# Kernel tuning notes

Measured on AMD Instinct MI355X. Metric: run time of the kernel, lower is better.

The kernel has to match this reference:

```python
import jax, jax.numpy as jnp
import numpy as np

B, C, H, W = 32, 256, 56, 56
G, K, RED = 2, 7, 4
BN_EPS = 1e-5


def _conv2d(x, w, pad, groups=1, bias=None):
    # x: (N, Cin, H, W), w: (Cout, Cin/groups, kh, kw)
    y = jax.lax.conv_general_dilated(
        x, w, window_strides=(1, 1), padding=[(pad, pad), (pad, pad)],
        dimension_numbers=("NCHW", "OIHW", "NCHW"), feature_group_count=groups)
    if bias is not None:
        y = y + bias[None, :, None, None]
    return y


def setup_inputs() -> dict:
    key = jax.random.key(0)
    ks = jax.random.split(key, 5)
    return {
        "x": jax.random.normal(ks[0], (B, C, H, W), jnp.float32),
        "w_dyn": jax.random.normal(ks[1], (G, C, K, K), jnp.float32) * 0.02,
        "proj1_w": jax.random.normal(ks[2], (C // RED, C, 3, 3), jnp.float32) * 0.02,
        "bn_gamma": jnp.ones((C // RED,), jnp.float32),
        "bn_beta": jnp.zeros((C // RED,), jnp.float32),
        "proj2_w": jax.random.normal(ks[3], (C * G, C // RED, 3, 3), jnp.float32) * 0.02,
        "proj2_b": jnp.zeros((C * G,), jnp.float32),
    }


def reference(x, w_dyn, proj1_w, bn_gamma, bn_beta, proj2_w, proj2_b):
    b, c, h, w = x.shape
    # AdaptiveAvgPool2d((K, K)); H, W divisible by K -> exact mean over (H//K, W//K) windows
    pooled = x.reshape(b, c, K, h // K, K, w // K).mean(axis=(3, 5))  # (B, C, K, K)
    # proj: Conv3x3 (no bias, BN follows) -> BN (inference: mean=0, var=1) -> GELU -> Conv3x3
    hmid = _conv2d(pooled, proj1_w, pad=1)
    hmid = hmid * (bn_gamma / jnp.sqrt(1.0 + BN_EPS))[None, :, None, None] + bn_beta[None, :, None, None]
    hmid = jax.nn.gelu(hmid, approximate=False)
    scale = _conv2d(hmid, proj2_w, pad=1, bias=proj2_b)  # (B, G*C, K, K)
    scale = jax.nn.softmax(scale.reshape(b, G, c, K, K), axis=1)
    # per-sample dynamic depthwise kernel: softmax-weighted mix of G kernel banks
    dyn_w = jnp.einsum("bgckl,gckl->bckl", scale, w_dyn)  # (B, C, K, K)
    # depthwise conv with per-sample weights: groups = B*C
    y = _conv2d(x.reshape(1, b * c, h, w), dyn_w.reshape(b * c, 1, K, K),
                pad=K // 2, groups=b * c)
    return y.reshape(b, c, h, w)
```

## Files before the change

kernel.cpp:

```cpp
#include <hip/hip_runtime.h>
#include <math.h>

#define BB 32
#define CC 256
#define HH 56
#define WW 56
#define KP 49
#define CMID 64
#define HW 3136

__global__ __launch_bounds__(256) void pre_kernel(const float* __restrict__ x,
                                                  const float* __restrict__ w1,
                                                  const float* __restrict__ w2,
                                                  float* __restrict__ pooled,
                                                  float* __restrict__ w1t,
                                                  float* __restrict__ w2t) {
    int bid = blockIdx.x;
    if (bid < 2048) {
        int wv = threadIdx.x >> 6, lane = threadIdx.x & 63;
        int g = bid * 4 + wv;
        if (lane < KP) {
            int ko = lane / 7, kw = lane - ko * 7;
            const float* base = x + (size_t)g * HW + (ko * 8) * WW + kw * 8;
            float s = 0.f;
            #pragma unroll
            for (int r = 0; r < 8; ++r) {
                float4 a = *(const float4*)(base + r * WW);
                float4 b4 = *(const float4*)(base + r * WW + 4);
                s += a.x + a.y + a.z + a.w + b4.x + b4.y + b4.z + b4.w;
            }
            pooled[(size_t)g * KP + lane] = s * (1.f / 64.f);
        }
        return;
    }
    __shared__ float t[64][65];
    int r = threadIdx.x >> 6, c = threadIdx.x & 63;
    if (bid < 2048 + 36) {
        int ct0 = (bid - 2048) * 64;
        #pragma unroll
        for (int i = 0; i < 16; ++i)
            t[r + 4 * i][c] = w1[(size_t)(r + 4 * i) * 2304 + ct0 + c];
        __syncthreads();
        #pragma unroll
        for (int i = 0; i < 16; ++i)
            w1t[(size_t)(ct0 + r + 4 * i) * 64 + c] = t[c][r + 4 * i];
    } else {
        int tt = bid - 2048 - 36;
        int co0 = (tt / 9) * 64, ct0 = (tt % 9) * 64;
        #pragma unroll
        for (int i = 0; i < 16; ++i)
            t[r + 4 * i][c] = w2[(size_t)(co0 + r + 4 * i) * 576 + ct0 + c];
        __syncthreads();
        #pragma unroll
        for (int i = 0; i < 16; ++i)
            w2t[(size_t)(ct0 + r + 4 * i) * 512 + co0 + c] = t[c][r + 4 * i];
    }
}

__global__ __launch_bounds__(1024) void conv1_kernel(const float* __restrict__ pooled,
                                                     const float* __restrict__ w1t,
                                                     const float* __restrict__ gamma,
                                                     const float* __restrict__ beta,
                                                     float* __restrict__ hmid) {
    int y = blockIdx.x, b = blockIdx.y;
    int wv = threadIdx.x >> 6, co = threadIdx.x & 63;
    __shared__ float red[16][7][64];
    float acc[7] = {0.f, 0.f, 0.f, 0.f, 0.f, 0.f, 0.f};
    const float* pb = pooled + (size_t)b * CC * KP;
    int cin0 = __builtin_amdgcn_readfirstlane(wv * 16);
    #pragma unroll 4
    for (int ci = 0; ci < 16; ++ci) {
        int cin = cin0 + ci;
        const float* prow_base = pb + cin * KP;
        const float* wbase = w1t + (size_t)(cin * 9) * 64 + co;
        #pragma unroll
        for (int ky = 0; ky < 3; ++ky) {
            int iy = y + ky - 1;
            if (0 <= iy && iy < 7) {
                float s[9];
                s[0] = 0.f; s[8] = 0.f;
                const float* pr = prow_base + iy * 7;
                #pragma unroll
                for (int j = 0; j < 7; ++j) s[j + 1] = pr[j];
                const float* wr = wbase + ky * 3 * 64;
                float w0 = wr[0], w1v = wr[64], w2v = wr[128];
                #pragma unroll
                for (int xx = 0; xx < 7; ++xx)
                    acc[xx] += s[xx] * w0 + s[xx + 1] * w1v + s[xx + 2] * w2v;
            }
        }
    }
    #pragma unroll
    for (int xx = 0; xx < 7; ++xx) red[wv][xx][co] = acc[xx];
    __syncthreads();
    if (threadIdx.x < 448) {
        int xx = threadIdx.x >> 6, c2 = threadIdx.x & 63;
        float tot = 0.f;
        #pragma unroll
        for (int w = 0; w < 16; ++w) tot += red[w][xx][c2];
        float bnscale = gamma[c2] * rsqrtf(1.f + 1e-5f);
        float h = tot * bnscale + beta[c2];
        float g = 0.5f * h * (1.f + erff(h * 0.70710678118654752440f));
        hmid[((size_t)b * CMID + c2) * KP + y * 7 + xx] = g;
    }
}

__global__ __launch_bounds__(1024) void conv2_kernel(const float* __restrict__ hmid,
                                                     const float* __restrict__ w2t,
                                                     const float* __restrict__ b2,
                                                     const float* __restrict__ wdyn,
                                                     float* __restrict__ dynw) {
    int y = blockIdx.x, b = blockIdx.y;
    int qq = threadIdx.x >> 8, co = threadIdx.x & 255;
    __shared__ float redA[4][7][256];
    __shared__ float redB[4][7][256];
    float a0[7] = {}, a1[7] = {};
    const float* hb = hmid + (size_t)b * CMID * KP;
    int cin0 = __builtin_amdgcn_readfirstlane(qq * 16);
    #pragma unroll 2
    for (int ci = 0; ci < 16; ++ci) {
        int cin = cin0 + ci;
        const float* hrow_base = hb + cin * KP;
        const float* wbase = w2t + (size_t)(cin * 9) * 512 + co;
        #pragma unroll
        for (int ky = 0; ky < 3; ++ky) {
            int iy = y + ky - 1;
            if (0 <= iy && iy < 7) {
                float s[9];
                s[0] = 0.f; s[8] = 0.f;
                const float* hr = hrow_base + iy * 7;
                #pragma unroll
                for (int j = 0; j < 7; ++j) s[j + 1] = hr[j];
                const float* wr = wbase + ky * 3 * 512;
                float wa0 = wr[0],    wb0 = wr[256];
                float wa1 = wr[512],  wb1 = wr[768];
                float wa2 = wr[1024], wb2 = wr[1280];
                #pragma unroll
                for (int xx = 0; xx < 7; ++xx) {
                    float v0 = s[xx], v1 = s[xx + 1], v2 = s[xx + 2];
                    a0[xx] += v0 * wa0 + v1 * wa1 + v2 * wa2;
                    a1[xx] += v0 * wb0 + v1 * wb1 + v2 * wb2;
                }
            }
        }
    }
    #pragma unroll
    for (int xx = 0; xx < 7; ++xx) { redA[qq][xx][co] = a0[xx]; redB[qq][xx][co] = a1[xx]; }
    __syncthreads();
    if (threadIdx.x < 256) {
        int c = threadIdx.x;
        float bias0 = b2[c], bias1 = b2[c + CC];
        const float* wd0 = wdyn + (size_t)c * KP + y * 7;
        const float* wd1 = wdyn + (size_t)(CC + c) * KP + y * 7;
        float* dw = dynw + ((size_t)(b * CC + c)) * KP + y * 7;
        #pragma unroll
        for (int xx = 0; xx < 7; ++xx) {
            float s0 = redA[0][xx][c] + redA[1][xx][c] + redA[2][xx][c] + redA[3][xx][c] + bias0;
            float s1 = redB[0][xx][c] + redB[1][xx][c] + redB[2][xx][c] + redB[3][xx][c] + bias1;
            float m = fmaxf(s0, s1);
            float e0 = expf(s0 - m), e1 = expf(s1 - m);
            dw[xx] = (e0 * wd0[xx] + e1 * wd1[xx]) / (e0 + e1);
        }
    }
}

__global__ __launch_bounds__(256, 4) void dwconv_kernel(const float* __restrict__ x,
                                                        const float* __restrict__ dynw,
                                                        float* __restrict__ out) {
    int tid = threadIdx.x & 63;
    int wv = threadIdx.x >> 6;
    int g = __builtin_amdgcn_readfirstlane(blockIdx.x * 4 + wv);

    const float* wp = dynw + (size_t)g * KP;
    float w[49];
    #pragma unroll
    for (int i = 0; i < 49; ++i) w[i] = wp[i];

    if (tid < 56) {
        int ty = tid / 7, tx = tid - ty * 7;
        int r0 = 7 * ty, c0 = 8 * tx;
        const float* xp = x + (size_t)g * HW;
        float acc[7][8] = {};
        #pragma unroll
        for (int ir = 0; ir < 13; ++ir) {
            int r = r0 + ir - 3;
            bool rowok = (unsigned)r < 56u;
            int rbase = r * WW;
            float rb[16];
            #pragma unroll
            for (int k = 0; k < 4; ++k) {
                int w0 = c0 - 4 + 4 * k;
                bool ok = rowok & ((unsigned)w0 < 56u);
                int off = ok ? (rbase + w0) : 0;
                float4 v = *(const float4*)(xp + off);
                if (!ok) v = make_float4(0.f, 0.f, 0.f, 0.f);
                rb[4 * k + 0] = v.x; rb[4 * k + 1] = v.y;
                rb[4 * k + 2] = v.z; rb[4 * k + 3] = v.w;
            }
            #pragma unroll
            for (int ky = 0; ky < 7; ++ky) {
                int oy = ir - ky;
                if (0 <= oy && oy < 7) {
                    #pragma unroll
                    for (int kx = 0; kx < 7; ++kx) {
                        float ww = w[ky * 7 + kx];
                        #pragma unroll
                        for (int ox = 0; ox < 8; ++ox)
                            acc[oy][ox] += rb[ox + 1 + kx] * ww;
                    }
                }
            }
        }
        float* op = out + (size_t)g * HW;
        #pragma unroll
        for (int oy = 0; oy < 7; ++oy) {
            float* orow = op + (r0 + oy) * WW + c0;
            *(float4*)(orow)     = make_float4(acc[oy][0], acc[oy][1], acc[oy][2], acc[oy][3]);
            *(float4*)(orow + 4) = make_float4(acc[oy][4], acc[oy][5], acc[oy][6], acc[oy][7]);
        }
    }
}

extern "C" void kernel_launch(void* const* d_in, const int* in_sizes, int n_in,
                              void* d_out, int out_size, void* d_ws, size_t ws_size,
                              hipStream_t stream) {
    const float* x     = (const float*)d_in[0];
    const float* wdyn  = (const float*)d_in[1];
    const float* w1    = (const float*)d_in[2];
    const float* gamma = (const float*)d_in[3];
    const float* beta  = (const float*)d_in[4];
    const float* w2    = (const float*)d_in[5];
    const float* b2    = (const float*)d_in[6];
    float* out = (float*)d_out;

    float* ws     = (float*)d_ws;
    float* pooled = ws;
    float* hmid   = ws + 401408;
    float* dynw   = ws + 501760;
    float* w1t    = ws + 903168;
    float* w2t    = ws + 1050624;

    pre_kernel   <<<dim3(2048 + 36 + 72),  256, 0, stream>>>(x, w1, w2, pooled, w1t, w2t);
    conv1_kernel <<<dim3(7, BB),          1024, 0, stream>>>(pooled, w1t, gamma, beta, hmid);
    conv2_kernel <<<dim3(7, BB),          1024, 0, stream>>>(hmid, w2t, b2, wdyn, dynw);
    dwconv_kernel<<<dim3(BB * CC / 4),     256, 0, stream>>>(x, dynw, out);
}
```

Baseline: 282.4 us.

## Fuse conv1 and conv2 into one kernel and split dwconv tiles across waves

Merges the two small 3x3 projection convolutions into one kernel. Each block recomputes the three hmid rows it needs (rows y-1..y+1) in shared memory, which removes the hmid global round trip and one launch at the cost of roughly 3x redundant conv1 work. Separately, the depthwise conv now splits each channel across two waves with 4-wide column tiles instead of 8. It double-buffers row loads against compute, which halves per-thread accumulators and doubles the number of waves, at the cost of more redundant halo loads.

```diff
diff --git a/kernel.cpp b/kernel.cpp
--- a/kernel.cpp
+++ b/kernel.cpp
@@ -57,95 +57,114 @@
     }
 }
 
-__global__ __launch_bounds__(1024) void conv1_kernel(const float* __restrict__ pooled,
-                                                     const float* __restrict__ w1t,
-                                                     const float* __restrict__ gamma,
-                                                     const float* __restrict__ beta,
-                                                     float* __restrict__ hmid) {
+__global__ __launch_bounds__(1024) void convfused_kernel(const float* __restrict__ pooled,
+                                                         const float* __restrict__ w1t,
+                                                         const float* __restrict__ gamma,
+                                                         const float* __restrict__ beta,
+                                                         const float* __restrict__ w2t,
+                                                         const float* __restrict__ b2,
+                                                         const float* __restrict__ wdyn,
+                                                         float* __restrict__ dynw) {
     int y = blockIdx.x, b = blockIdx.y;
-    int wv = threadIdx.x >> 6, co = threadIdx.x & 63;
-    __shared__ float red[16][7][64];
-    float acc[7] = {0.f, 0.f, 0.f, 0.f, 0.f, 0.f, 0.f};
-    const float* pb = pooled + (size_t)b * CC * KP;
-    int cin0 = __builtin_amdgcn_readfirstlane(wv * 16);
-    #pragma unroll 4
-    for (int ci = 0; ci < 16; ++ci) {
-        int cin = cin0 + ci;
-        const float* prow_base = pb + cin * KP;
-        const float* wbase = w1t + (size_t)(cin * 9) * 64 + co;
-        #pragma unroll
-        for (int ky = 0; ky < 3; ++ky) {
-            int iy = y + ky - 1;
-            if (0 <= iy && iy < 7) {
+    __shared__ float red16[16][3][7][64];
+    __shared__ float hmid3[CMID][22];
+
+    {
+        int wv = threadIdx.x >> 6, co = threadIdx.x & 63;
+        float acc3[3][7] = {};
+        const float* pb = pooled + (size_t)b * CC * KP;
+        int cin0 = __builtin_amdgcn_readfirstlane(wv * 16);
+        #pragma unroll 2
+        for (int ci = 0; ci < 16; ++ci) {
+            int cin = cin0 + ci;
+            const float* prow_base = pb + cin * KP;
+            const float* wbase = w1t + (size_t)(cin * 9) * 64 + co;
+            float wv0[3], wv1[3], wv2[3];
+            #pragma unroll
+            for (int ky = 0; ky < 3; ++ky) {
+                const float* wr = wbase + ky * 192;
+                wv0[ky] = wr[0]; wv1[ky] = wr[64]; wv2[ky] = wr[128];
+            }
+            #pragma unroll
+            for (int rr = 0; rr < 5; ++rr) {
+                int iy = y - 2 + rr;
                 float s[9];
                 s[0] = 0.f; s[8] = 0.f;
-                const float* pr = prow_base + iy * 7;
+                if (0 <= iy && iy < 7) {
+                    const float* pr = prow_base + iy * 7;
+                    #pragma unroll
+                    for (int j = 0; j < 7; ++j) s[j + 1] = pr[j];
+                } else {
+                    #pragma unroll
+                    for (int j = 0; j < 7; ++j) s[j + 1] = 0.f;
+                }
                 #pragma unroll
-                for (int j = 0; j < 7; ++j) s[j + 1] = pr[j];
-                const float* wr = wbase + ky * 3 * 64;
-                float w0 = wr[0], w1v = wr[64], w2v = wr[128];
-                #pragma unroll
-                for (int xx = 0; xx < 7; ++xx)
-                    acc[xx] += s[xx] * w0 + s[xx + 1] * w1v + s[xx + 2] * w2v;
-            }
-        }
-    }
-    #pragma unroll
-    for (int xx = 0; xx < 7; ++xx) red[wv][xx][co] = acc[xx];
+                for (int ky = 0; ky < 3; ++ky) {
+                    int d = rr - ky;
+                    if (0 <= d && d < 3) {
+                        #pragma unroll
+                        for (int xx = 0; xx < 7; ++xx)
+                            acc3[d][xx] += s[xx] * wv0[ky] + s[xx + 1] * wv1[ky]
+                                         + s[xx + 2] * wv2[ky];
+                    }
+                }
+            }
+        }
+        #pragma unroll
+        for (int d = 0; d < 3; ++d)
+            #pragma unroll
+            for (int xx = 0; xx < 7; ++xx)
+                red16[wv][d][xx][co] = acc3[d][xx];
+    }
     __syncthreads();
-    if (threadIdx.x < 448) {
-        int xx = threadIdx.x >> 6, c2 = threadIdx.x & 63;
+    for (int idx = threadIdx.x; idx < 3 * 7 * 64; idx += 1024) {
+        int c2 = idx & 63, rest = idx >> 6;
+        int d = rest / 7, xx = rest - d * 7;
         float tot = 0.f;
         #pragma unroll
-        for (int w = 0; w < 16; ++w) tot += red[w][xx][c2];
+        for (int w = 0; w < 16; ++w) tot += red16[w][d][xx][c2];
         float bnscale = gamma[c2] * rsqrtf(1.f + 1e-5f);
         float h = tot * bnscale + beta[c2];
         float g = 0.5f * h * (1.f + erff(h * 0.70710678118654752440f));
-        hmid[((size_t)b * CMID + c2) * KP + y * 7 + xx] = g;
-    }
-}
-
-__global__ __launch_bounds__(1024) void conv2_kernel(const float* __restrict__ hmid,
-                                                     const float* __restrict__ w2t,
-                                                     const float* __restrict__ b2,
-                                                     const float* __restrict__ wdyn,
-                                                     float* __restrict__ dynw) {
-    int y = blockIdx.x, b = blockIdx.y;
-    int qq = threadIdx.x >> 8, co = threadIdx.x & 255;
-    __shared__ float redA[4][7][256];
-    __shared__ float redB[4][7][256];
-    float a0[7] = {}, a1[7] = {};
-    const float* hb = hmid + (size_t)b * CMID * KP;
-    int cin0 = __builtin_amdgcn_readfirstlane(qq * 16);
-    #pragma unroll 2
-    for (int ci = 0; ci < 16; ++ci) {
-        int cin = cin0 + ci;
-        const float* hrow_base = hb + cin * KP;
-        const float* wbase = w2t + (size_t)(cin * 9) * 512 + co;
-        #pragma unroll
-        for (int ky = 0; ky < 3; ++ky) {
-            int iy = y + ky - 1;
-            if (0 <= iy && iy < 7) {
-                float s[9];
-                s[0] = 0.f; s[8] = 0.f;
-                const float* hr = hrow_base + iy * 7;
-                #pragma unroll
-                for (int j = 0; j < 7; ++j) s[j + 1] = hr[j];
-                const float* wr = wbase + ky * 3 * 512;
-                float wa0 = wr[0],    wb0 = wr[256];
-                float wa1 = wr[512],  wb1 = wr[768];
-                float wa2 = wr[1024], wb2 = wr[1280];
-                #pragma unroll
-                for (int xx = 0; xx < 7; ++xx) {
-                    float v0 = s[xx], v1 = s[xx + 1], v2 = s[xx + 2];
-                    a0[xx] += v0 * wa0 + v1 * wa1 + v2 * wa2;
-                    a1[xx] += v0 * wb0 + v1 * wb1 + v2 * wb2;
+        hmid3[c2][d * 7 + xx] = g;
+    }
+    __syncthreads();
+
+    float (*redA)[7][256] = (float (*)[7][256])(&red16[0][0][0][0]);
+    float (*redB)[7][256] = (float (*)[7][256])(&red16[0][0][0][0] + 4 * 7 * 256);
+    {
+        int qq = threadIdx.x >> 8, co = threadIdx.x & 255;
+        float a0[7] = {}, a1[7] = {};
+        int cin0 = __builtin_amdgcn_readfirstlane(qq * 16);
+        #pragma unroll 2
+        for (int ci = 0; ci < 16; ++ci) {
+            int cin = cin0 + ci;
+            const float* wbase = w2t + (size_t)(cin * 9) * 512 + co;
+            #pragma unroll
+            for (int ky = 0; ky < 3; ++ky) {
+                int iy = y + ky - 1;
+                if (0 <= iy && iy < 7) {
+                    float s[9];
+                    s[0] = 0.f; s[8] = 0.f;
+                    const float* hr = &hmid3[cin][ky * 7];
+                    #pragma unroll
+                    for (int j = 0; j < 7; ++j) s[j + 1] = hr[j];
+                    const float* wr = wbase + ky * 3 * 512;
+                    float wa0 = wr[0],    wb0 = wr[256];
+                    float wa1 = wr[512],  wb1 = wr[768];
+                    float wa2 = wr[1024], wb2 = wr[1280];
+                    #pragma unroll
+                    for (int xx = 0; xx < 7; ++xx) {
+                        float v0 = s[xx], v1 = s[xx + 1], v2 = s[xx + 2];
+                        a0[xx] += v0 * wa0 + v1 * wa1 + v2 * wa2;
+                        a1[xx] += v0 * wb0 + v1 * wb1 + v2 * wb2;
+                    }
                 }
             }
         }
-    }
-    #pragma unroll
-    for (int xx = 0; xx < 7; ++xx) { redA[qq][xx][co] = a0[xx]; redB[qq][xx][co] = a1[xx]; }
+        #pragma unroll
+        for (int xx = 0; xx < 7; ++xx) { redA[qq][xx][co] = a0[xx]; redB[qq][xx][co] = a1[xx]; }
+    }
     __syncthreads();
     if (threadIdx.x < 256) {
         int c = threadIdx.x;
@@ -164,12 +183,13 @@
     }
 }
 
-__global__ __launch_bounds__(256, 4) void dwconv_kernel(const float* __restrict__ x,
-                                                        const float* __restrict__ dynw,
-                                                        float* __restrict__ out) {
+__global__ __launch_bounds__(256) void dwconv_kernel(const float* __restrict__ x,
+                                                     const float* __restrict__ dynw,
+                                                     float* __restrict__ out) {
     int tid = threadIdx.x & 63;
     int wv = threadIdx.x >> 6;
-    int g = __builtin_amdgcn_readfirstlane(blockIdx.x * 4 + wv);
+    int p = wv >> 1, sub = wv & 1;
+    int g = __builtin_amdgcn_readfirstlane(blockIdx.x * 2 + p);
 
     const float* wp = dynw + (size_t)g * KP;
     float w[49];
@@ -178,46 +198,56 @@
 
     if (tid < 56) {
         int ty = tid / 7, tx = tid - ty * 7;
-        int r0 = 7 * ty, c0 = 8 * tx;
+        int r0 = 7 * ty;
+        int c0 = 28 * sub + 4 * tx;
         const float* xp = x + (size_t)g * HW;
-        float acc[7][8] = {};
-        #pragma unroll
-        for (int ir = 0; ir < 13; ++ir) {
-            int r = r0 + ir - 3;
-            bool rowok = (unsigned)r < 56u;
-            int rbase = r * WW;
-            float rb[16];
-            #pragma unroll
-            for (int k = 0; k < 4; ++k) {
-                int w0 = c0 - 4 + 4 * k;
-                bool ok = rowok & ((unsigned)w0 < 56u);
-                int off = ok ? (rbase + w0) : 0;
-                float4 v = *(const float4*)(xp + off);
-                if (!ok) v = make_float4(0.f, 0.f, 0.f, 0.f);
-                rb[4 * k + 0] = v.x; rb[4 * k + 1] = v.y;
-                rb[4 * k + 2] = v.z; rb[4 * k + 3] = v.w;
-            }
-            #pragma unroll
-            for (int ky = 0; ky < 7; ++ky) {
-                int oy = ir - ky;
-                if (0 <= oy && oy < 7) {
-                    #pragma unroll
-                    for (int kx = 0; kx < 7; ++kx) {
-                        float ww = w[ky * 7 + kx];
-                        #pragma unroll
-                        for (int ox = 0; ox < 8; ++ox)
-                            acc[oy][ox] += rb[ox + 1 + kx] * ww;
-                    }
-                }
-            }
-        }
+        float acc[7][4] = {};
+        float rbA[12], rbB[12];
+
+#define LOADR(IR, RB) { \
+        int r = r0 + (IR) - 3; \
+        bool rowok = (unsigned)r < 56u; \
+        int rbase = r * WW; \
+        _Pragma("unroll") \
+        for (int k = 0; k < 3; ++k) { \
+            int w0c = c0 - 4 + 4 * k; \
+            bool ok = rowok && ((unsigned)w0c < 56u); \
+            int off = ok ? (rbase + w0c) : 0; \
+            float4 v = *(const float4*)(xp + off); \
+            if (!ok) v = make_float4(0.f, 0.f, 0.f, 0.f); \
+            RB[4*k+0] = v.x; RB[4*k+1] = v.y; RB[4*k+2] = v.z; RB[4*k+3] = v.w; \
+        } }
+
+#define COMPR(IR, RB) { \
+        _Pragma("unroll") \
+        for (int ky = 0; ky < 7; ++ky) { \
+            int oy = (IR) - ky; \
+            if (0 <= oy && oy < 7) { \
+                _Pragma("unroll") \
+                for (int kx = 0; kx < 7; ++kx) { \
+                    float ww = w[ky * 7 + kx]; \
+                    _Pragma("unroll") \
+                    for (int ox = 0; ox < 4; ++ox) \
+                        acc[oy][ox] += RB[ox + kx + 1] * ww; \
+                } } } }
+
+        LOADR(0, rbA)
+        #pragma unroll
+        for (int ii = 0; ii < 6; ++ii) {
+            LOADR(2 * ii + 1, rbB)
+            COMPR(2 * ii,     rbA)
+            LOADR(2 * ii + 2, rbA)
+            COMPR(2 * ii + 1, rbB)
+        }
+        COMPR(12, rbA)
+#undef LOADR
+#undef COMPR
+
         float* op = out + (size_t)g * HW;
         #pragma unroll
-        for (int oy = 0; oy < 7; ++oy) {
-            float* orow = op + (r0 + oy) * WW + c0;
-            *(float4*)(orow)     = make_float4(acc[oy][0], acc[oy][1], acc[oy][2], acc[oy][3]);
-            *(float4*)(orow + 4) = make_float4(acc[oy][4], acc[oy][5], acc[oy][6], acc[oy][7]);
-        }
+        for (int oy = 0; oy < 7; ++oy)
+            *(float4*)(op + (r0 + oy) * WW + c0) =
+                make_float4(acc[oy][0], acc[oy][1], acc[oy][2], acc[oy][3]);
     }
 }
 
@@ -235,13 +265,12 @@
 
     float* ws     = (float*)d_ws;
     float* pooled = ws;
-    float* hmid   = ws + 401408;
     float* dynw   = ws + 501760;
     float* w1t    = ws + 903168;
     float* w2t    = ws + 1050624;
 
-    pre_kernel   <<<dim3(2048 + 36 + 72),  256, 0, stream>>>(x, w1, w2, pooled, w1t, w2t);
-    conv1_kernel <<<dim3(7, BB),          1024, 0, stream>>>(pooled, w1t, gamma, beta, hmid);
-    conv2_kernel <<<dim3(7, BB),          1024, 0, stream>>>(hmid, w2t, b2, wdyn, dynw);
-    dwconv_kernel<<<dim3(BB * CC / 4),     256, 0, stream>>>(x, dynw, out);
-}
+    pre_kernel      <<<dim3(2048 + 36 + 72),  256, 0, stream>>>(x, w1, w2, pooled, w1t, w2t);
+    convfused_kernel<<<dim3(7, BB),          1024, 0, stream>>>(pooled, w1t, gamma, beta,
+                                                               w2t, b2, wdyn, dynw);
+    dwconv_kernel   <<<dim3(BB * CC / 2),     256, 0, stream>>>(x, dynw, out);
+}
```

Measured after the change: 325.8 us. 1.15x slower.
